# Optimization experiments

Measured on AMD Instinct MI355X. Metric: run time of the kernel, lower is better.

The kernel has to match this reference:

```python
import jax, jax.numpy as jnp
import numpy as np

HIDDEN = 2048
NUM_HEADS = 16
HEAD_SIZE = HIDDEN // NUM_HEADS  # 128
SEQ = 2048
BATCH = 2


def alibi_causal_bias(seq_len: int, num_heads: int) -> jnp.ndarray:
    """[1, H, S, S] bias: -(i-j)*slope for j<=i, -inf for j>i (per source mask)."""
    i = jnp.arange(seq_len)[:, None]
    j = jnp.arange(seq_len)[None, :]
    dist = -(i - j).astype(jnp.float32)            # 0 on diag, -(i-j) below
    causal = jnp.where(j > i, -jnp.inf, 0.0)
    base = jnp.where(j > i, 0.0, dist) + causal     # [S, S]
    if num_heads <= 8:
        slopes = jnp.asarray([1.0 / 2**k for k in range(num_heads)], jnp.float32)
    else:
        slopes = jnp.asarray([1.0 / 2**(k / 2) for k in range(num_heads)], jnp.float32)
    # NOTE: source multiplies the mask (including -inf part) by the slope;
    # -inf * positive slope is still -inf, so applying slopes to the finite
    # part and adding -inf causal term is equivalent.
    return slopes[None, :, None, None] * dist[None, None] * (j <= i)[None, None] + causal[None, None]


def setup_inputs() -> dict:
    key = jax.random.key(0)
    ks = jax.random.split(key, 3)
    sd = 1.0 / np.sqrt(HIDDEN)
    return {
        "x": jax.random.normal(ks[0], (BATCH, SEQ, HIDDEN), jnp.float32),
        "Wqkv": jax.random.normal(ks[1], (HIDDEN, 3 * HIDDEN), jnp.float32) * sd,
        "bqkv": jnp.zeros((3 * HIDDEN,), jnp.float32),
        "Wo": jax.random.normal(ks[2], (HIDDEN, HIDDEN), jnp.float32) * sd,
        "bo": jnp.zeros((HIDDEN,), jnp.float32),
    }


def reference(x, Wqkv, bqkv, Wo, bo):
    b, s, h = x.shape
    scale = 1.0 / np.sqrt(HEAD_SIZE)
    qkv = x @ Wqkv + bqkv                                   # [b, s, 3h]
    q, k, v = jnp.split(qkv, 3, axis=-1)
    def heads(t):
        return t.reshape(b, s, NUM_HEADS, HEAD_SIZE).transpose(0, 2, 1, 3)
    q, k, v = heads(q), heads(k), heads(v)                  # [b, H, s, d]
    scores = jnp.einsum("bhid,bhjd->bhij", q, k) * scale
    scores = scores + alibi_causal_bias(s, NUM_HEADS)
    attn = jax.nn.softmax(scores, axis=-1)                  # dropout=0 (eval)
    out = jnp.einsum("bhij,bhjd->bhid", attn, v)            # [b, H, s, d]
    out = out.transpose(0, 2, 1, 3).reshape(b, s, NUM_HEADS * HEAD_SIZE)
    return out @ Wo + bo
```

## Files before the change

### kernel.cpp

```cpp
#include <hip/hip_runtime.h>

typedef __attribute__((ext_vector_type(4))) float f32x4;
typedef __attribute__((ext_vector_type(8))) __bf16 bf16x8;
typedef unsigned short u16;

#define GAS(p) ((const __attribute__((address_space(1))) void*)(p))
#define LAS(p) ((__attribute__((address_space(3))) void*)(p))

__device__ __forceinline__ u16 f32_to_bf16(float f) {
  unsigned u = __builtin_bit_cast(unsigned, f);
  u += 0x7FFFu + ((u >> 16) & 1u);
  return (u16)(u >> 16);
}

__global__ __launch_bounds__(256) void k_convert(const float* __restrict__ X,
                                                 u16* __restrict__ Y, int n4) {
  int i = blockIdx.x * 256 + threadIdx.x;
  if (i >= n4) return;
  float4 v = ((const float4*)X)[i];
  ushort4 r;
  r.x = f32_to_bf16(v.x); r.y = f32_to_bf16(v.y);
  r.z = f32_to_bf16(v.z); r.w = f32_to_bf16(v.w);
  ((ushort4*)Y)[i] = r;
}

__global__ __launch_bounds__(256) void k_transpose_w(const float* __restrict__ W,
                                                     u16* __restrict__ WT,
                                                     int K, int N) {
  __shared__ float tile[32][33];
  int n0 = blockIdx.x * 32, k0 = blockIdx.y * 32;
  int tx = threadIdx.x & 31, ty = threadIdx.x >> 5;
#pragma unroll
  for (int r = 0; r < 4; ++r)
    tile[ty + r * 8][tx] = W[(long)(k0 + ty + r * 8) * N + n0 + tx];
  __syncthreads();
#pragma unroll
  for (int r = 0; r < 4; ++r)
    WT[(long)(n0 + ty + r * 8) * K + k0 + tx] = f32_to_bf16(tile[tx][ty + r * 8]);
}

__global__ __launch_bounds__(256) void k_transpose_v(const u16* __restrict__ V,
                                                     u16* __restrict__ VT) {
  __shared__ u16 tile[32][34];
  int s0 = blockIdx.x * 32, d0 = blockIdx.y * 32, bh = blockIdx.z;
  int tx = threadIdx.x & 31, ty = threadIdx.x >> 5;
  const u16* Vb = V + (long)bh * 2048 * 128;
  u16* VTb = VT + (long)bh * 128 * 2048;
#pragma unroll
  for (int r = 0; r < 4; ++r)
    tile[ty + r * 8][tx] = Vb[(long)(s0 + ty + r * 8) * 128 + d0 + tx];
  __syncthreads();
#pragma unroll
  for (int r = 0; r < 4; ++r)
    VTb[(long)(d0 + ty + r * 8) * 2048 + s0 + tx] = tile[tx][ty + r * 8];
}

template <int EPI>
__global__ __launch_bounds__(256, 3) void k_gemm(
    const u16* __restrict__ A, const u16* __restrict__ BT,
    const float* __restrict__ bias,
    u16* __restrict__ Qo, u16* __restrict__ Ko, u16* __restrict__ Vo,
    float* __restrict__ Cout, int M, int N, int K) {
  __shared__ alignas(16) u16 AS[3][128 * 32];
  __shared__ alignas(16) u16 BS[3][128 * 32];
  const int wave = threadIdx.x >> 6, lane = threadIdx.x & 63;
  const int wr = wave >> 1, wc = wave & 1;
  const int l15 = lane & 15, l4 = lane >> 4;
  const int srow = lane >> 2;
  const int sslot = (lane & 3) ^ ((srow >> 1) & 3);

  const int nwg = gridDim.x;
  const int swz = ((int)blockIdx.x & 7) * (nwg >> 3) + ((int)blockIdx.x >> 3);
  const int mt = M >> 7;
  const int bm = swz % mt, bn = swz / mt;
  const int brow = bm * 128, bcol = bn * 128;
  const int NT = K >> 5;

  const u16* aBase = A + (long)(brow + wave * 16 + srow) * K + sslot * 8;
  const u16* bBase = BT + (long)(bcol + wave * 16 + srow) * K + sslot * 8;
  const long K64 = (long)K * 64;

  auto stage = [&](int t, int buf) {
    const long t32 = (long)t * 32;
    __builtin_amdgcn_global_load_lds(GAS(aBase + t32),
                                     LAS(&AS[buf][wave * 512]), 16, 0, 0);
    __builtin_amdgcn_global_load_lds(GAS(aBase + t32 + K64),
                                     LAS(&AS[buf][(wave + 4) * 512]), 16, 0, 0);
    __builtin_amdgcn_global_load_lds(GAS(bBase + t32),
                                     LAS(&BS[buf][wave * 512]), 16, 0, 0);
    __builtin_amdgcn_global_load_lds(GAS(bBase + t32 + K64),
                                     LAS(&BS[buf][(wave + 4) * 512]), 16, 0, 0);
  };

  const f32x4 fzero = {0.f, 0.f, 0.f, 0.f};
  f32x4 acc[4][4];
#pragma unroll
  for (int m = 0; m < 4; ++m)
#pragma unroll
    for (int n = 0; n < 4; ++n) acc[m][n] = fzero;

  const int rkey = (l15 >> 1) & 3;
  auto compute = [&](int buf) {
    const u16* Ac = &AS[buf][0];
    const u16* Bc = &BS[buf][0];
    bf16x8 afr[4], bfr[4];
#pragma unroll
    for (int f = 0; f < 4; ++f) {
      const int Ra = wr * 64 + f * 16 + l15;
      afr[f] = *(const bf16x8*)(Ac + Ra * 32 + ((l4 ^ rkey) * 8));
      const int Rb = wc * 64 + f * 16 + l15;
      bfr[f] = *(const bf16x8*)(Bc + Rb * 32 + ((l4 ^ rkey) * 8));
    }
    __builtin_amdgcn_s_setprio(1);
#pragma unroll
    for (int m = 0; m < 4; ++m)
#pragma unroll
      for (int n = 0; n < 4; ++n)
        acc[m][n] = __builtin_amdgcn_mfma_f32_16x16x32_bf16(afr[m], bfr[n],
                                                            acc[m][n], 0, 0, 0);
    __builtin_amdgcn_s_setprio(0);
  };

  stage(0, 0);
  stage(1, 1);
  int bufc = 0;
  for (int t = 0; t < NT - 1; ++t) {
    asm volatile("s_waitcnt vmcnt(4)" ::: "memory");
    __builtin_amdgcn_s_barrier();
    if (t + 2 < NT) {
      int bufn = bufc + 2;
      if (bufn >= 3) bufn -= 3;
      stage(t + 2, bufn);
    }
    compute(bufc);
    ++bufc;
    if (bufc == 3) bufc = 0;
  }
  asm volatile("s_waitcnt vmcnt(0)" ::: "memory");
  __builtin_amdgcn_s_barrier();
  compute(bufc);

  if (EPI == 0) {
    const int which = bcol >> 11;
    u16* dst = (which == 0) ? Qo : (which == 1) ? Ko : Vo;
    const int cbase = bcol & 2047;
#pragma unroll
    for (int n = 0; n < 4; ++n) {
      const int col = cbase + wc * 64 + n * 16 + l15;
      const int h = col >> 7, d = col & 127;
      const float bv = bias[bcol + wc * 64 + n * 16 + l15];
#pragma unroll
      for (int m = 0; m < 4; ++m) {
#pragma unroll
        for (int r = 0; r < 4; ++r) {
          const int row = brow + wr * 64 + m * 16 + l4 * 4 + r;
          const int bb = row >> 11, s = row & 2047;
          dst[(((long)(bb * 16 + h)) * 2048 + s) * 128 + d] =
              f32_to_bf16(acc[m][n][r] + bv);
        }
      }
    }
  } else {
#pragma unroll
    for (int m = 0; m < 4; ++m)
#pragma unroll
      for (int r = 0; r < 4; ++r) {
        const int row = brow + wr * 64 + m * 16 + l4 * 4 + r;
#pragma unroll
        for (int n = 0; n < 4; ++n) {
          const int col = bcol + wc * 64 + n * 16 + l15;
          Cout[(long)row * N + col] = acc[m][n][r] + bias[col];
        }
      }
  }
}

__global__ __launch_bounds__(256, 4) void k_attn(const u16* __restrict__ Q,
                                                 const u16* __restrict__ Kp,
                                                 const u16* __restrict__ VT,
                                                 u16* __restrict__ Oa) {
  __shared__ alignas(16) u16 Kl[2][64 * 128];
  __shared__ alignas(16) u16 Vl[2][128 * 64];
  __shared__ alignas(16) u16 Pl[4][16 * 64];
  const int b = blockIdx.x;
  const int bh = b & 31;
  const int qt = 31 - (b >> 5);
  const int bb = bh >> 4, h = bh & 15;
  const int wave = threadIdx.x >> 6, lane = threadIdx.x & 63;
  const int l15 = lane & 15, l4 = lane >> 4;
  const int l7 = lane & 7, l8 = lane >> 3;
  const float LOG2E = 1.4426950408889634f;
  const float scale = 0.08838834764831845f * LOG2E;
  const float slope = exp2f(-0.5f * (float)h) * LOG2E;

  const int q0 = qt * 64 + wave * 16;
  const u16* Qb = Q + ((long)bh * 2048 + q0 + l15) * 128;
  bf16x8 qf[4];
#pragma unroll
  for (int kk = 0; kk < 4; ++kk) qf[kk] = *(const bf16x8*)(Qb + kk * 32 + l4 * 8);

  const u16* Kb = Kp + (long)bh * 2048 * 128;
  const u16* VTb = VT + (long)bh * 128 * 2048;

  auto stageK = [&](int jt, int buf) {
#pragma unroll
    for (int g = 0; g < 4; ++g) {
      const int wcc = g * 4 + wave;
      const int row = wcc * 4 + l4;
      const u16* src = Kb + (long)(jt * 64 + row) * 128 + ((l15 ^ (row & 7)) * 8);
      __builtin_amdgcn_global_load_lds(GAS(src), LAS(&Kl[buf][wcc * 512]), 16, 0, 0);
    }
  };
  auto stageV = [&](int jt, int buf) {
#pragma unroll
    for (int g = 0; g < 4; ++g) {
      const int wcc = g * 4 + wave;
      const int d = wcc * 8 + l8;
      const u16* src = VTb + (long)d * 2048 + jt * 64 + ((l7 ^ l8) * 8);
      __builtin_amdgcn_global_load_lds(GAS(src), LAS(&Vl[buf][wcc * 512]), 16, 0, 0);
    }
  };

  float rs[4];
  f32x4 O[8];
  const f32x4 fzero = {0.f, 0.f, 0.f, 0.f};
#pragma unroll
  for (int r = 0; r < 4; ++r) rs[r] = 0.f;
#pragma unroll
  for (int nb = 0; nb < 8; ++nb) O[nb] = fzero;

  u16* Pw = Pl[wave];
  const int irow = q0 + l4 * 4;
  const int sw = l15 & 7;

  stageK(0, 0);
  stageV(0, 0);
  __syncthreads();

  for (int jt = 0; jt <= qt; ++jt) {
    const int cur = jt & 1;
    if (jt < qt) {
      stageK(jt + 1, cur ^ 1);
      stageV(jt + 1, cur ^ 1);
    }
    const u16* Kc = Kl[cur];
    const u16* Vc = Vl[cur];
    const int j0 = jt * 64;
#pragma unroll
    for (int cb = 0; cb < 4; ++cb) {
      f32x4 sa = fzero;
      const u16* kp = Kc + (cb * 16 + l15) * 128;
#pragma unroll
      for (int kk = 0; kk < 4; ++kk) {
        bf16x8 kf = *(const bf16x8*)(kp + (((kk * 4 + l4) ^ sw) * 8));
        sa = __builtin_amdgcn_mfma_f32_16x16x32_bf16(qf[kk], kf, sa, 0, 0, 0);
      }
      const int j = j0 + cb * 16 + l15;
#pragma unroll
      for (int r = 0; r < 4; ++r) {
        int i = irow + r;
        float s = sa[r] * scale - slope * (float)(i - j);
        float p = __builtin_amdgcn_exp2f((j <= i) ? s : -1e30f);
        rs[r] += p;
        int rloc = l4 * 4 + r;
        int cbyte = (cb * 16 + l15) * 2;
        *(u16*)((char*)Pw + rloc * 128 + (cbyte ^ ((rloc & 7) << 4))) =
            f32_to_bf16(p);
      }
    }
    bf16x8 pf0 = *(const bf16x8*)((char*)Pw + l15 * 128 +
                                  ((l4 * 16) ^ ((l15 & 7) << 4)));
    bf16x8 pf1 = *(const bf16x8*)((char*)Pw + l15 * 128 +
                                  ((64 + l4 * 16) ^ ((l15 & 7) << 4)));
#pragma unroll
    for (int nb = 0; nb < 8; ++nb) {
      const u16* vp = Vc + (nb * 16 + l15) * 64;
      bf16x8 v0 = *(const bf16x8*)(vp + ((l4 ^ sw) * 8));
      bf16x8 v1 = *(const bf16x8*)(vp + (((4 + l4) ^ sw) * 8));
      O[nb] = __builtin_amdgcn_mfma_f32_16x16x32_bf16(pf0, v0, O[nb], 0, 0, 0);
      O[nb] = __builtin_amdgcn_mfma_f32_16x16x32_bf16(pf1, v1, O[nb], 0, 0, 0);
    }
    __syncthreads();
  }
#pragma unroll
  for (int r = 0; r < 4; ++r) {
    float v = rs[r];
    v += __shfl_xor(v, 1);
    v += __shfl_xor(v, 2);
    v += __shfl_xor(v, 4);
    v += __shfl_xor(v, 8);
    float inv = 1.f / v;
    int i = irow + r;
    u16* op = Oa + ((long)bb * 2048 + i) * 2048 + h * 128;
#pragma unroll
    for (int nb = 0; nb < 8; ++nb) op[nb * 16 + l15] = f32_to_bf16(O[nb][r] * inv);
  }
}

extern "C" void kernel_launch(void* const* d_in, const int* in_sizes, int n_in,
                              void* d_out, int out_size, void* d_ws, size_t ws_size,
                              hipStream_t stream) {
  const float* x = (const float*)d_in[0];
  const float* Wqkv = (const float*)d_in[1];
  const float* bqkv = (const float*)d_in[2];
  const float* Wo = (const float*)d_in[3];
  const float* bo = (const float*)d_in[4];
  float* out = (float*)d_out;

  char* ws = (char*)d_ws;
  u16* xb = (u16*)(ws);
  u16* VTb = (u16*)(ws);
  u16* WqkvT = (u16*)(ws + 16777216);
  u16* attn_out = (u16*)(ws + 16777216);
  u16* WoT = (u16*)(ws + 16777216 + 25165824);
  u16* Qb = (u16*)(ws + 50331648);
  u16* Kb = (u16*)(ws + 67108864);
  u16* Vb = (u16*)(ws + 83886080);

  k_convert<<<8192, 256, 0, stream>>>(x, xb, 8388608 / 4);
  k_transpose_w<<<dim3(192, 64), 256, 0, stream>>>(Wqkv, WqkvT, 2048, 6144);
  k_transpose_w<<<dim3(64, 64), 256, 0, stream>>>(Wo, WoT, 2048, 2048);
  k_gemm<0><<<dim3(1536), 256, 0, stream>>>(xb, WqkvT, bqkv, Qb, Kb, Vb,
                                            nullptr, 4096, 6144, 2048);
  k_transpose_v<<<dim3(64, 4, 32), 256, 0, stream>>>(Vb, VTb);
  k_attn<<<dim3(1024), 256, 0, stream>>>(Qb, Kb, VTb, attn_out);
  k_gemm<1><<<dim3(512), 256, 0, stream>>>(attn_out, WoT, bo, nullptr,
                                           nullptr, nullptr, out, 4096, 2048,
                                           2048);
}
```

Measured before the change: 271.9 us.

## Single-buffer attention K/V LDS and reorder query-tile block scheduling

Drops the double-buffered K/V shared-memory tiles in favour of single buffers, which roughly halves LDS per block (about 66KB to 34KB) so more blocks can be resident per CU. Each iteration now finishes compute, syncs, loads the next tile, waits on vmcnt and syncs again, so load latency is no longer overlapped with compute inside a block. It also replaces the strictly descending query-tile order with a serpentine grouping of tiles to balance the causal workload across blocks differently.

```diff
diff --git a/kernel.cpp b/kernel.cpp
--- a/kernel.cpp
+++ b/kernel.cpp
@@ -179,12 +179,14 @@
                                                  const u16* __restrict__ Kp,
                                                  const u16* __restrict__ VT,
                                                  u16* __restrict__ Oa) {
-  __shared__ alignas(16) u16 Kl[2][64 * 128];
-  __shared__ alignas(16) u16 Vl[2][128 * 64];
+  __shared__ alignas(16) u16 Kl[64 * 128];
+  __shared__ alignas(16) u16 Vl[128 * 64];
   __shared__ alignas(16) u16 Pl[4][16 * 64];
   const int b = blockIdx.x;
   const int bh = b & 31;
-  const int qt = 31 - (b >> 5);
+  const int g = b >> 5;
+  const int gj = g >> 3, gk = g & 7;
+  const int qt = gj * 8 + ((gj & 1) ? (7 - gk) : gk);
   const int bb = bh >> 4, h = bh & 15;
   const int wave = threadIdx.x >> 6, lane = threadIdx.x & 63;
   const int l15 = lane & 15, l4 = lane >> 4;
@@ -202,22 +204,22 @@
   const u16* Kb = Kp + (long)bh * 2048 * 128;
   const u16* VTb = VT + (long)bh * 128 * 2048;
 
-  auto stageK = [&](int jt, int buf) {
-#pragma unroll
-    for (int g = 0; g < 4; ++g) {
-      const int wcc = g * 4 + wave;
+  auto stageK = [&](int jt) {
+#pragma unroll
+    for (int gg = 0; gg < 4; ++gg) {
+      const int wcc = gg * 4 + wave;
       const int row = wcc * 4 + l4;
       const u16* src = Kb + (long)(jt * 64 + row) * 128 + ((l15 ^ (row & 7)) * 8);
-      __builtin_amdgcn_global_load_lds(GAS(src), LAS(&Kl[buf][wcc * 512]), 16, 0, 0);
+      __builtin_amdgcn_global_load_lds(GAS(src), LAS(&Kl[wcc * 512]), 16, 0, 0);
     }
   };
-  auto stageV = [&](int jt, int buf) {
-#pragma unroll
-    for (int g = 0; g < 4; ++g) {
-      const int wcc = g * 4 + wave;
+  auto stageV = [&](int jt) {
+#pragma unroll
+    for (int gg = 0; gg < 4; ++gg) {
+      const int wcc = gg * 4 + wave;
       const int d = wcc * 8 + l8;
       const u16* src = VTb + (long)d * 2048 + jt * 64 + ((l7 ^ l8) * 8);
-      __builtin_amdgcn_global_load_lds(GAS(src), LAS(&Vl[buf][wcc * 512]), 16, 0, 0);
+      __builtin_amdgcn_global_load_lds(GAS(src), LAS(&Vl[wcc * 512]), 16, 0, 0);
     }
   };
 
@@ -233,23 +235,17 @@
   const int irow = q0 + l4 * 4;
   const int sw = l15 & 7;
 
-  stageK(0, 0);
-  stageV(0, 0);
+  stageK(0);
+  stageV(0);
+  asm volatile("s_waitcnt vmcnt(0)" ::: "memory");
   __syncthreads();
 
   for (int jt = 0; jt <= qt; ++jt) {
-    const int cur = jt & 1;
-    if (jt < qt) {
-      stageK(jt + 1, cur ^ 1);
-      stageV(jt + 1, cur ^ 1);
-    }
-    const u16* Kc = Kl[cur];
-    const u16* Vc = Vl[cur];
     const int j0 = jt * 64;
 #pragma unroll
     for (int cb = 0; cb < 4; ++cb) {
       f32x4 sa = fzero;
-      const u16* kp = Kc + (cb * 16 + l15) * 128;
+      const u16* kp = Kl + (cb * 16 + l15) * 128;
 #pragma unroll
       for (int kk = 0; kk < 4; ++kk) {
         bf16x8 kf = *(const bf16x8*)(kp + (((kk * 4 + l4) ^ sw) * 8));
@@ -274,13 +270,19 @@
                                   ((64 + l4 * 16) ^ ((l15 & 7) << 4)));
 #pragma unroll
     for (int nb = 0; nb < 8; ++nb) {
-      const u16* vp = Vc + (nb * 16 + l15) * 64;
+      const u16* vp = Vl + (nb * 16 + l15) * 64;
       bf16x8 v0 = *(const bf16x8*)(vp + ((l4 ^ sw) * 8));
       bf16x8 v1 = *(const bf16x8*)(vp + (((4 + l4) ^ sw) * 8));
       O[nb] = __builtin_amdgcn_mfma_f32_16x16x32_bf16(pf0, v0, O[nb], 0, 0, 0);
       O[nb] = __builtin_amdgcn_mfma_f32_16x16x32_bf16(pf1, v1, O[nb], 0, 0, 0);
     }
-    __syncthreads();
+    if (jt < qt) {
+      __syncthreads();
+      stageK(jt + 1);
+      stageV(jt + 1);
+      asm volatile("s_waitcnt vmcnt(0)" ::: "memory");
+      __syncthreads();
+    }
   }
 #pragma unroll
   for (int r = 0; r < 4; ++r) {
```

New measurement: 316.1 us. 1.16x slower.
